# Performance work log

Measured on AMD Instinct MI355X. Metric: run time of the kernel, lower is better.

Reference implementation:

```python
import jax, jax.numpy as jnp
import numpy as np

GAMMA = 1.0 / 512.0  # RBF bandwidth, 1/d_feat


def _rbf_kernel(X, Z, gamma):
    # X: [N, d], Z: [M, d] -> K: [N, M], K[i,j] = exp(-gamma * ||x_i - z_j||^2)
    xn = jnp.sum(X * X, axis=1, keepdims=True)        # [N, 1]
    zn = jnp.sum(Z * Z, axis=1, keepdims=True).T      # [1, M]
    sq = xn + zn - 2.0 * (X @ Z.T)                    # [N, M]
    return jnp.exp(-gamma * jnp.maximum(sq, 0.0))


def setup_inputs() -> dict:
    key = jax.random.key(0)
    k1, k2, k3, k4, k5 = jax.random.split(key, 5)
    N, d, M = 8192, 512, 4096
    inputs = jax.random.normal(k1, (M, d), dtype=jnp.float32)
    X = jax.random.normal(k2, (N, d), dtype=jnp.float32)
    # SVM labels in {-1, +1}
    Y = jnp.where(jax.random.uniform(k3, (N, 1)) > 0.5, 1.0, -1.0).astype(jnp.float32)
    a = jax.random.normal(k4, (N, 1), dtype=jnp.float32) * 0.1
    b = jax.random.normal(k5, (1, 1), dtype=jnp.float32)
    return {"inputs": inputs, "X": X, "Y": Y, "a": a, "b": b}


def reference(inputs, X, Y, a, b):
    # K: [N, M]; weighted sum over support vectors N, then add bias, transpose.
    K = _rbf_kernel(X, inputs, GAMMA)                 # [N, M]
    s = jnp.sum(a * Y * K, axis=0)                    # [M]
    out = (s + b)                                     # [1, M] via broadcast with [1,1]
    return out.T                                      # [M, 1]
```

## Files before the change

### kernel.cpp

```cpp
#include <hip/hip_runtime.h>
#include <hip/hip_bf16.h>
#include <stdint.h>

#define C2EXP (-0.0028179443441958f)

static constexpr int N_SV = 8192;
static constexpr int M_Q  = 4096;
static constexpr int DIM  = 512;

typedef __bf16 bf16x8 __attribute__((ext_vector_type(8)));
typedef float  f32x4  __attribute__((ext_vector_type(4)));

#define GLB const __attribute__((address_space(1))) void
#define LDS __attribute__((address_space(3))) void

__global__ __launch_bounds__(256) void svm_prep(
    const float* __restrict__ Z, const float* __restrict__ X,
    const float* __restrict__ Y, const float* __restrict__ a,
    const float* __restrict__ b,
    __bf16* __restrict__ Xb, __bf16* __restrict__ Zb,
    float* __restrict__ xn, float* __restrict__ zn, float* __restrict__ w,
    float* __restrict__ out)
{
    const int r = blockIdx.x * 4 + (threadIdx.x >> 6);
    const int t = threadIdx.x & 63;
    const float* src;
    __bf16* dst;
    if (r < N_SV) { src = X + (size_t)r * DIM; dst = Xb + (size_t)r * DIM; }
    else          { src = Z + (size_t)(r - N_SV) * DIM; dst = Zb + (size_t)(r - N_SV) * DIM; }

    const float4* row4 = (const float4*)src;
    float4 v0 = row4[t];
    float4 v1 = row4[t + 64];

    float s = v0.x*v0.x + v0.y*v0.y + v0.z*v0.z + v0.w*v0.w
            + v1.x*v1.x + v1.y*v1.y + v1.z*v1.z + v1.w*v1.w;

    __bf16 h0[4] = {(__bf16)v0.x, (__bf16)v0.y, (__bf16)v0.z, (__bf16)v0.w};
    __bf16 h1[4] = {(__bf16)v1.x, (__bf16)v1.y, (__bf16)v1.z, (__bf16)v1.w};
    uint2 b0, b1;
    __builtin_memcpy(&b0, h0, 8);
    __builtin_memcpy(&b1, h1, 8);
    ((uint2*)dst)[t]      = b0;
    ((uint2*)dst)[t + 64] = b1;

    #pragma unroll
    for (int o = 32; o > 0; o >>= 1) s += __shfl_xor(s, o);

    if (t == 0) {
        if (r < N_SV) { xn[r] = s; w[r] = a[r] * Y[r]; }
        else          { int m = r - N_SV; zn[m] = s; out[m] = b[0]; }
    }
}

__global__ __launch_bounds__(512, 2) void svm_main(
    const __bf16* __restrict__ Xb, const __bf16* __restrict__ Zb,
    const float* __restrict__ xn, const float* __restrict__ zn,
    const float* __restrict__ w, float* __restrict__ out)
{
    __shared__ char Sh[65536];

    const int tid  = threadIdx.x;
    const int lane = tid & 63;
    const int wid  = tid >> 6;
    const int wr   = wid >> 2;
    const int wc   = wid & 3;

    const int iBase = blockIdx.y * 256;
    const int jBase = blockIdx.x * 256;

    f32x4 acc[8][4];
    #pragma unroll
    for (int m = 0; m < 8; ++m)
        #pragma unroll
        for (int n = 0; n < 4; ++n)
            acc[m][n] = (f32x4)(0.0f);

    auto stage = [&](const __bf16* Mb, int rowBase, int t, int op) {
        char* dst0 = (char*)Sh + ((t & 1) * 32768) + op * 16384 + tid * 16;
        const __bf16* src0 = Mb
            + (size_t)(rowBase + (lane & 15)) * DIM + t * 32 + (lane >> 4) * 8;
        #pragma unroll
        for (int s = 0; s < 2; ++s) {
            const __bf16* src = src0 + (size_t)((s * 8 + wid) * 16) * DIM;
            __builtin_amdgcn_global_load_lds((GLB*)src, (LDS*)(dst0 + s * 8192),
                                             16, 0, 0);
        }
    };

    stage(Xb, iBase, 0, 0);
    stage(Zb, jBase, 0, 1);
    stage(Zb, jBase, 1, 1);
    asm volatile("s_waitcnt vmcnt(2)" ::: "memory");
    __builtin_amdgcn_s_barrier();

    bf16x8 af[4], bfr[4];

    #pragma unroll
    for (int t = 0; t < 16; ++t) {
        const int buf = t & 1;
        const char* Ab = (const char*)Sh + buf * 32768 + lane * 16;

        #pragma unroll
        for (int m = 0; m < 4; ++m)
            af[m] = *(const bf16x8*)(Ab + (wr * 8 + m) * 1024);
        #pragma unroll
        for (int n = 0; n < 4; ++n)
            bfr[n] = *(const bf16x8*)(Ab + 16384 + (wc * 4 + n) * 1024);
        if (t + 1 < 16) stage(Xb, iBase, t + 1, 0);
        __builtin_amdgcn_s_barrier();
        asm volatile("s_waitcnt lgkmcnt(0)" ::: "memory");
        __builtin_amdgcn_sched_barrier(0);
        __builtin_amdgcn_s_setprio(1);
        #pragma unroll
        for (int m = 0; m < 4; ++m)
            #pragma unroll
            for (int n = 0; n < 4; ++n)
                acc[m][n] = __builtin_amdgcn_mfma_f32_16x16x32_bf16(
                    af[m], bfr[n], acc[m][n], 0, 0, 0);
        __builtin_amdgcn_s_setprio(0);
        __builtin_amdgcn_s_barrier();

        #pragma unroll
        for (int m = 0; m < 4; ++m)
            af[m] = *(const bf16x8*)(Ab + (wr * 8 + 4 + m) * 1024);
        if (t + 2 < 16) stage(Zb, jBase, t + 2, 1);
        __builtin_amdgcn_s_barrier();
        asm volatile("s_waitcnt lgkmcnt(0)" ::: "memory");
        __builtin_amdgcn_sched_barrier(0);
        __builtin_amdgcn_s_setprio(1);
        #pragma unroll
        for (int m = 0; m < 4; ++m)
            #pragma unroll
            for (int n = 0; n < 4; ++n)
                acc[4 + m][n] = __builtin_amdgcn_mfma_f32_16x16x32_bf16(
                    af[m], bfr[n], acc[4 + m][n], 0, 0, 0);
        __builtin_amdgcn_s_setprio(0);

        if (t < 14) {
            asm volatile("s_waitcnt vmcnt(2)" ::: "memory");
            __builtin_amdgcn_s_barrier();
        } else if (t == 14) {
            asm volatile("s_waitcnt vmcnt(0)" ::: "memory");
            __builtin_amdgcn_s_barrier();
        }
    }

    const int rg   = lane >> 4;
    const int lcol = lane & 15;

    float znv[4];
    #pragma unroll
    for (int n = 0; n < 4; ++n)
        znv[n] = zn[jBase + wc * 64 + n * 16 + lcol];

    float cs[4] = {0.f, 0.f, 0.f, 0.f};
    #pragma unroll
    for (int m = 0; m < 8; ++m) {
        float wv[4], xv[4];
        #pragma unroll
        for (int r = 0; r < 4; ++r) {
            const int i = iBase + wr * 128 + m * 16 + rg * 4 + r;
            wv[r] = w[i];
            xv[r] = xn[i];
        }
        #pragma unroll
        for (int n = 0; n < 4; ++n)
            #pragma unroll
            for (int r = 0; r < 4; ++r) {
                float d = xv[r] + znv[n] - 2.0f * acc[m][n][r];
                d = fmaxf(d, 0.0f);
                cs[n] += wv[r] * exp2f(C2EXP * d);
            }
    }

    #pragma unroll
    for (int n = 0; n < 4; ++n) {
        const int j = jBase + wc * 64 + n * 16 + lcol;
        float c = cs[n];
        c += __shfl_xor(c, 16);
        c += __shfl_xor(c, 32);
        if (lane < 16) atomicAdd(out + j, c);
    }
}

extern "C" void kernel_launch(void* const* d_in, const int* in_sizes, int n_in,
                              void* d_out, int out_size, void* d_ws, size_t ws_size,
                              hipStream_t stream)
{
    const float* Z = (const float*)d_in[0];
    const float* X = (const float*)d_in[1];
    const float* Y = (const float*)d_in[2];
    const float* a = (const float*)d_in[3];
    const float* b = (const float*)d_in[4];
    float* out = (float*)d_out;

    char* ws = (char*)d_ws;
    __bf16* Xb = (__bf16*)ws;
    __bf16* Zb = (__bf16*)(ws + 8ull * 1024 * 1024);
    float*  xn = (float*)(ws + 12ull * 1024 * 1024);
    float*  zn = xn + N_SV;
    float*  w  = zn + M_Q;

    svm_prep<<<(N_SV + M_Q) / 4, 256, 0, stream>>>(Z, X, Y, a, b, Xb, Zb, xn, zn, w, out);
    svm_main<<<dim3(M_Q / 256, N_SV / 256), 512, 0, stream>>>(Xb, Zb, xn, zn, w, out);
}
```

Measured before the change: 119.9 us.

## Pre-pack bf16 operands into MFMA-tile-contiguous layout for contiguous LDS staging

The prep kernel now writes X and Z in bf16 as 1 KB blocks, one per 16-row by 32-column tile, indexed by k-step and row panel. Each block is laid out in exactly the order the main kernel's global_load_lds expects. The main kernel's staging then reads fully contiguous 16-byte-per-thread spans instead of strided row fragments. This cuts scattered global accesses and address math in the GEMM loop. In exchange the prep kernel uses a new block decomposition with a shared-memory reduction for the row norms, and its writes are less sequential per row.

```diff
diff --git a/kernel.cpp b/kernel.cpp
--- a/kernel.cpp
+++ b/kernel.cpp
@@ -7,6 +7,9 @@
 static constexpr int N_SV = 8192;
 static constexpr int M_Q  = 4096;
 static constexpr int DIM  = 512;
+static constexpr int NP_A = N_SV / 16;
+static constexpr int NP_B = M_Q / 16;
+static constexpr int NKT  = DIM / 32;
 
 typedef __bf16 bf16x8 __attribute__((ext_vector_type(8)));
 typedef float  f32x4  __attribute__((ext_vector_type(4)));
@@ -18,43 +21,55 @@
     const float* __restrict__ Z, const float* __restrict__ X,
     const float* __restrict__ Y, const float* __restrict__ a,
     const float* __restrict__ b,
-    __bf16* __restrict__ Xb, __bf16* __restrict__ Zb,
+    __bf16* __restrict__ Xp, __bf16* __restrict__ Zp,
     float* __restrict__ xn, float* __restrict__ zn, float* __restrict__ w,
     float* __restrict__ out)
 {
-    const int r = blockIdx.x * 4 + (threadIdx.x >> 6);
-    const int t = threadIdx.x & 63;
-    const float* src;
-    __bf16* dst;
-    if (r < N_SV) { src = X + (size_t)r * DIM; dst = Xb + (size_t)r * DIM; }
-    else          { src = Z + (size_t)(r - N_SV) * DIM; dst = Zb + (size_t)(r - N_SV) * DIM; }
-
-    const float4* row4 = (const float4*)src;
-    float4 v0 = row4[t];
-    float4 v1 = row4[t + 64];
-
-    float s = v0.x*v0.x + v0.y*v0.y + v0.z*v0.z + v0.w*v0.w
-            + v1.x*v1.x + v1.y*v1.y + v1.z*v1.z + v1.w*v1.w;
-
-    __bf16 h0[4] = {(__bf16)v0.x, (__bf16)v0.y, (__bf16)v0.z, (__bf16)v0.w};
-    __bf16 h1[4] = {(__bf16)v1.x, (__bf16)v1.y, (__bf16)v1.z, (__bf16)v1.w};
-    uint2 b0, b1;
-    __builtin_memcpy(&b0, h0, 8);
-    __builtin_memcpy(&b1, h1, 8);
-    ((uint2*)dst)[t]      = b0;
-    ((uint2*)dst)[t + 64] = b1;
-
-    #pragma unroll
-    for (int o = 32; o > 0; o >>= 1) s += __shfl_xor(s, o);
-
-    if (t == 0) {
-        if (r < N_SV) { xn[r] = s; w[r] = a[r] * Y[r]; }
-        else          { int m = r - N_SV; zn[m] = s; out[m] = b[0]; }
+    __shared__ float part[4][16];
+
+    const int tid  = threadIdx.x;
+    const int lane = tid & 63;
+    const int wv   = tid >> 6;
+    const int pb   = blockIdx.x;
+    const bool isA = (pb < NP_A);
+    const int p    = isA ? pb : pb - NP_A;
+    const float* src = (isA ? X : Z) + (size_t)p * 16 * DIM;
+    __bf16* dst  = isA ? Xp : Zp;
+    const int np = isA ? NP_A : NP_B;
+
+    const int row = lane & 15;
+    const int ch  = lane >> 4;
+
+    float s = 0.0f;
+    #pragma unroll
+    for (int f = 0; f < 4; ++f) {
+        const int kt = wv * 4 + f;
+        const float4* rp = (const float4*)(src + (size_t)row * DIM + kt * 32 + ch * 8);
+        float4 v0 = rp[0], v1 = rp[1];
+        s += v0.x*v0.x + v0.y*v0.y + v0.z*v0.z + v0.w*v0.w
+           + v1.x*v1.x + v1.y*v1.y + v1.z*v1.z + v1.w*v1.w;
+        __bf16 h[8] = {(__bf16)v0.x, (__bf16)v0.y, (__bf16)v0.z, (__bf16)v0.w,
+                       (__bf16)v1.x, (__bf16)v1.y, (__bf16)v1.z, (__bf16)v1.w};
+        uint4 bits;
+        __builtin_memcpy(&bits, h, 16);
+        *(uint4*)((char*)dst + (((size_t)kt * np + p) << 10) + lane * 16) = bits;
+    }
+
+    s += __shfl_xor(s, 16);
+    s += __shfl_xor(s, 32);
+    if (lane < 16) part[wv][lane] = s;
+    __syncthreads();
+
+    if (tid < 16) {
+        const float t = part[0][tid] + part[1][tid] + part[2][tid] + part[3][tid];
+        const int r = p * 16 + tid;
+        if (isA) { xn[r] = t; w[r] = a[r] * Y[r]; }
+        else     { zn[r] = t; out[r] = b[0]; }
     }
 }
 
 __global__ __launch_bounds__(512, 2) void svm_main(
-    const __bf16* __restrict__ Xb, const __bf16* __restrict__ Zb,
+    const __bf16* __restrict__ Xp, const __bf16* __restrict__ Zp,
     const float* __restrict__ xn, const float* __restrict__ zn,
     const float* __restrict__ w, float* __restrict__ out)
 {
@@ -68,6 +83,8 @@
 
     const int iBase = blockIdx.y * 256;
     const int jBase = blockIdx.x * 256;
+    const int pbA   = blockIdx.y * 16;
+    const int pbB   = blockIdx.x * 16;
 
     f32x4 acc[8][4];
     #pragma unroll
@@ -76,28 +93,24 @@
         for (int n = 0; n < 4; ++n)
             acc[m][n] = (f32x4)(0.0f);
 
-    auto stage = [&](const __bf16* Mb, int rowBase, int t, int op) {
+    auto stage = [&](const __bf16* Mp, int pb16, int t, int op, int np) {
         char* dst0 = (char*)Sh + ((t & 1) * 32768) + op * 16384 + tid * 16;
-        const __bf16* src0 = Mb
-            + (size_t)(rowBase + (lane & 15)) * DIM + t * 32 + (lane >> 4) * 8;
-        #pragma unroll
-        for (int s = 0; s < 2; ++s) {
-            const __bf16* src = src0 + (size_t)((s * 8 + wid) * 16) * DIM;
-            __builtin_amdgcn_global_load_lds((GLB*)src, (LDS*)(dst0 + s * 8192),
-                                             16, 0, 0);
-        }
+        const char* s0 = (const char*)Mp + (((size_t)t * np + pb16) << 10) + tid * 16;
+        __builtin_amdgcn_global_load_lds((GLB*)s0, (LDS*)dst0, 16, 0, 0);
+        __builtin_amdgcn_global_load_lds((GLB*)(s0 + 8192), (LDS*)(dst0 + 8192),
+                                         16, 0, 0);
     };
 
-    stage(Xb, iBase, 0, 0);
-    stage(Zb, jBase, 0, 1);
-    stage(Zb, jBase, 1, 1);
+    stage(Xp, pbA, 0, 0, NP_A);
+    stage(Zp, pbB, 0, 1, NP_B);
+    stage(Zp, pbB, 1, 1, NP_B);
     asm volatile("s_waitcnt vmcnt(2)" ::: "memory");
     __builtin_amdgcn_s_barrier();
 
     bf16x8 af[4], bfr[4];
 
     #pragma unroll
-    for (int t = 0; t < 16; ++t) {
+    for (int t = 0; t < NKT; ++t) {
         const int buf = t & 1;
         const char* Ab = (const char*)Sh + buf * 32768 + lane * 16;
 
@@ -107,7 +120,7 @@
         #pragma unroll
         for (int n = 0; n < 4; ++n)
             bfr[n] = *(const bf16x8*)(Ab + 16384 + (wc * 4 + n) * 1024);
-        if (t + 1 < 16) stage(Xb, iBase, t + 1, 0);
+        if (t + 1 < NKT) stage(Xp, pbA, t + 1, 0, NP_A);
         __builtin_amdgcn_s_barrier();
         asm volatile("s_waitcnt lgkmcnt(0)" ::: "memory");
         __builtin_amdgcn_sched_barrier(0);
@@ -124,7 +137,7 @@
         #pragma unroll
         for (int m = 0; m < 4; ++m)
             af[m] = *(const bf16x8*)(Ab + (wr * 8 + 4 + m) * 1024);
-        if (t + 2 < 16) stage(Zb, jBase, t + 2, 1);
+        if (t + 2 < NKT) stage(Zp, pbB, t + 2, 1, NP_B);
         __builtin_amdgcn_s_barrier();
         asm volatile("s_waitcnt lgkmcnt(0)" ::: "memory");
         __builtin_amdgcn_sched_barrier(0);
@@ -137,10 +150,10 @@
                     af[m], bfr[n], acc[4 + m][n], 0, 0, 0);
         __builtin_amdgcn_s_setprio(0);
 
-        if (t < 14) {
+        if (t < NKT - 2) {
             asm volatile("s_waitcnt vmcnt(2)" ::: "memory");
             __builtin_amdgcn_s_barrier();
-        } else if (t == 14) {
+        } else if (t == NKT - 2) {
             asm volatile("s_waitcnt vmcnt(0)" ::: "memory");
             __builtin_amdgcn_s_barrier();
         }
@@ -196,12 +209,12 @@
     float* out = (float*)d_out;
 
     char* ws = (char*)d_ws;
-    __bf16* Xb = (__bf16*)ws;
-    __bf16* Zb = (__bf16*)(ws + 8ull * 1024 * 1024);
+    __bf16* Xp = (__bf16*)ws;
+    __bf16* Zp = (__bf16*)(ws + 8ull * 1024 * 1024);
     float*  xn = (float*)(ws + 12ull * 1024 * 1024);
     float*  zn = xn + N_SV;
     float*  w  = zn + M_Q;
 
-    svm_prep<<<(N_SV + M_Q) / 4, 256, 0, stream>>>(Z, X, Y, a, b, Xb, Zb, xn, zn, w, out);
-    svm_main<<<dim3(M_Q / 256, N_SV / 256), 512, 0, stream>>>(Xb, Zb, xn, zn, w, out);
+    svm_prep<<<NP_A + NP_B, 256, 0, stream>>>(Z, X, Y, a, b, Xp, Zp, xn, zn, w, out);
+    svm_main<<<dim3(M_Q / 256, N_SV / 256), 512, 0, stream>>>(Xp, Zp, xn, zn, w, out);
 }
```

Measured after the change: 111.3 us. 1.08x faster.
